# Performance work log

Measured on AMD Instinct MI355X. Metric: run time of the kernel, lower is better.

The kernel has to match this reference:

```python
import jax, jax.numpy as jnp
import numpy as np

B, S, D = 1, 2048, 2048
NH, NKV, HD = 32, 8, 64
EPS = 1e-5
SCALE = float(HD) ** 0.5


def _rope(x, cos, sin):
    # x: [b, h, s, hd]; cos/sin: [s, hd//2]; interleaved-pair rotary (executorch style)
    xr = x[..., 0::2]
    xi = x[..., 1::2]
    c = cos[None, None, :, :]
    s = sin[None, None, :, :]
    out_r = xr * c - xi * s
    out_i = xr * s + xi * c
    return jnp.stack([out_r, out_i], axis=-1).reshape(x.shape)


def _rmsnorm(x, w):
    var = jnp.mean(x * x, axis=-1, keepdims=True)
    return x * jax.lax.rsqrt(var + EPS) * w


def setup_inputs() -> dict:
    key = jax.random.key(0)
    ks = jax.random.split(key, 6)
    hidden_states = jax.random.normal(ks[0], (B, S, D), dtype=jnp.float32)
    # standard Llama rope tables, theta=10000
    inv_freq = 1.0 / (10000.0 ** (np.arange(0, HD, 2, dtype=np.float32) / HD))
    t = np.arange(S, dtype=np.float32)
    ang = np.outer(t, inv_freq)  # [S, HD//2]
    freqs_cos = jnp.asarray(np.cos(ang), dtype=jnp.float32)
    freqs_sin = jnp.asarray(np.sin(ang), dtype=jnp.float32)
    # additive causal mask [1,1,S,S]
    causal = jnp.tril(jnp.ones((S, S), dtype=bool))
    atten_mask = jnp.where(causal, 0.0, -1e9).astype(jnp.float32)[None, None]
    sd = 1.0 / np.sqrt(D)
    wq = jax.random.normal(ks[1], (NH * HD, D), dtype=jnp.float32) * sd
    wk = jax.random.normal(ks[2], (NKV * HD, D), dtype=jnp.float32) * sd
    wv = jax.random.normal(ks[3], (NKV * HD, D), dtype=jnp.float32) * sd
    wo = jax.random.normal(ks[4], (D, NH * HD), dtype=jnp.float32) * sd
    q_norm_w = jnp.ones((HD,), dtype=jnp.float32)
    k_norm_w = jnp.ones((HD,), dtype=jnp.float32)
    return dict(hidden_states=hidden_states, freqs_cos=freqs_cos, freqs_sin=freqs_sin,
                atten_mask=atten_mask, wq=wq, wk=wk, wv=wv, wo=wo,
                q_norm_w=q_norm_w, k_norm_w=k_norm_w)


def reference(hidden_states, freqs_cos, freqs_sin, atten_mask, wq, wk, wv, wo, q_norm_w, k_norm_w):
    b, s, _ = hidden_states.shape
    n_rep = NH // NKV
    # fused QKV projections (Linear: x @ W.T)
    q = (hidden_states @ wq.T).reshape(b, s, NH, HD).transpose(0, 2, 1, 3)   # [b,nh,s,hd]
    k = (hidden_states @ wk.T).reshape(b, s, NKV, HD).transpose(0, 2, 1, 3)  # [b,nkv,s,hd]
    v = (hidden_states @ wv.T).reshape(b, s, NKV, HD).transpose(0, 2, 1, 3)
    # RoPE, then QK RMSNorm (qk_norm_before_rope=False)
    q = _rope(q, freqs_cos, freqs_sin)
    k = _rope(k, freqs_cos, freqs_sin)
    q = _rmsnorm(q, q_norm_w)
    k = _rmsnorm(k, k_norm_w)
    # no KV cache (prefill): kh = k^T, vh = v, then GQA repeat
    kh = jnp.repeat(k, n_rep, axis=1)  # [b,nh,s,hd]
    vh = jnp.repeat(v, n_rep, axis=1)
    attn = jnp.einsum('bhqd,bhkd->bhqk', q, kh) / SCALE
    attn = jax.nn.softmax(attn + atten_mask, axis=-1)
    y = jnp.einsum('bhqk,bhkd->bhqd', attn, vh)
    y = y.transpose(0, 2, 1, 3).reshape(b, s, NH * HD)
    y = y @ wo.T
    # module returns (y, [kh], [vh]); kh stored transposed (b,nh,hd,s)
    return (y, kh.transpose(0, 1, 3, 2), vh)
```

## Files before the change

kernel.cpp:

```cpp
#include <hip/hip_runtime.h>
#include <cstdint>
#include <cstddef>

#define S_   2048
#define D_   2048
#define NH_  32
#define NKV_ 8
#define HD_  64

using bf16x8 = __attribute__((ext_vector_type(8))) __bf16;
using f32x4  = __attribute__((ext_vector_type(4))) float;

#define AS_GLOBAL(p) (const __attribute__((address_space(1))) void*)(p)
#define AS_LDS(p)    (__attribute__((address_space(3))) void*)(p)

__global__ __launch_bounds__(256) void cvt_all(
    const float* __restrict__ hs, const float* __restrict__ wq,
    const float* __restrict__ wk, const float* __restrict__ wv,
    const float* __restrict__ wo,
    __bf16* __restrict__ hs_bf, __bf16* __restrict__ wq_bf,
    __bf16* __restrict__ wk_bf, __bf16* __restrict__ wv_bf,
    __bf16* __restrict__ wo_bf) {
  int i = blockIdx.x * 256 + threadIdx.x;
  const float* src; __bf16* dst; int base;
  if (i < 1048576)      { src = hs; dst = hs_bf; base = 0; }
  else if (i < 2097152) { src = wq; dst = wq_bf; base = 1048576; }
  else if (i < 2359296) { src = wk; dst = wk_bf; base = 2097152; }
  else if (i < 2621440) { src = wv; dst = wv_bf; base = 2359296; }
  else                  { src = wo; dst = wo_bf; base = 2621440; }
  i -= base;
  const float4 v = reinterpret_cast<const float4*>(src)[i];
  __bf16 t[4] = {(__bf16)v.x, (__bf16)v.y, (__bf16)v.z, (__bf16)v.w};
  reinterpret_cast<uint2*>(dst)[i] = *reinterpret_cast<uint2*>(t);
}

__device__ __forceinline__ void gemm_compute_step(
    const char* ldsA, const char* ldsB, f32x4 (&acc)[4][4],
    int l15, int lg, int wm, int wn) {
  bf16x8 af[4][2], bfr[4][2];
#pragma unroll
  for (int f = 0; f < 4; ++f) {
    const int arow = wm*64 + f*16 + l15;
    const int brow = wn*64 + f*16 + l15;
#pragma unroll
    for (int ks = 0; ks < 2; ++ks) {
      af[f][ks] = *reinterpret_cast<const bf16x8*>(
          ldsA + arow*128 + (((ks*4 + lg) ^ (arow & 7)) << 4));
      bfr[f][ks] = *reinterpret_cast<const bf16x8*>(
          ldsB + brow*128 + (((ks*4 + lg) ^ (brow & 7)) << 4));
    }
  }
#pragma unroll
  for (int mf = 0; mf < 4; ++mf)
#pragma unroll
    for (int nf = 0; nf < 4; ++nf) {
      acc[mf][nf] = __builtin_amdgcn_mfma_f32_16x16x32_bf16(
          af[mf][0], bfr[nf][0], acc[mf][nf], 0, 0, 0);
      acc[mf][nf] = __builtin_amdgcn_mfma_f32_16x16x32_bf16(
          af[mf][1], bfr[nf][1], acc[mf][nf], 0, 0, 0);
    }
}

__device__ __forceinline__ void gemm_tile_128(
    const __bf16* __restrict__ A, const __bf16* __restrict__ B,
    float* __restrict__ C, int K, int N, int m0, int n0) {
  __shared__ __align__(16) char lds[2][32768];
  const int tid = threadIdx.x;
  const int l = tid & 63;
  const int w = tid >> 6;
  const int l15 = l & 15, lg = l >> 4;
  const int wm = w >> 1, wn = w & 1;

  f32x4 acc[4][4] = {};

  const int srow   = tid >> 3;
  const int schunk = (tid & 7) ^ (srow & 7);
  const __bf16* gA = A + (size_t)(m0 + srow) * K + schunk * 8;
  const __bf16* gB = B + (size_t)(n0 + srow) * K + schunk * 8;
  const int ldst = tid * 16;
  const int nt = K >> 6;

#pragma unroll
  for (int i = 0; i < 4; ++i) {
    __builtin_amdgcn_global_load_lds(AS_GLOBAL(gA + (size_t)i*32*K),
                                     AS_LDS(&lds[0][i*4096 + ldst]), 16, 0, 0);
    __builtin_amdgcn_global_load_lds(AS_GLOBAL(gB + (size_t)i*32*K),
                                     AS_LDS(&lds[0][16384 + i*4096 + ldst]), 16, 0, 0);
  }
  __syncthreads();

  int cur = 0;
  for (int t = 0; t < nt; ++t) {
    if (t + 1 < nt) {
      const int k0 = (t + 1) * 64;
      char* dA = &lds[cur ^ 1][0];
      char* dB = &lds[cur ^ 1][16384];
#pragma unroll
      for (int i = 0; i < 4; ++i) {
        __builtin_amdgcn_global_load_lds(AS_GLOBAL(gA + (size_t)i*32*K + k0),
                                         AS_LDS(dA + i*4096 + ldst), 16, 0, 0);
        __builtin_amdgcn_global_load_lds(AS_GLOBAL(gB + (size_t)i*32*K + k0),
                                         AS_LDS(dB + i*4096 + ldst), 16, 0, 0);
      }
    }
    gemm_compute_step(&lds[cur][0], &lds[cur][16384], acc, l15, lg, wm, wn);
    __syncthreads();
    cur ^= 1;
  }

#pragma unroll
  for (int mf = 0; mf < 4; ++mf)
#pragma unroll
    for (int nf = 0; nf < 4; ++nf)
#pragma unroll
      for (int r = 0; r < 4; ++r)
        C[(size_t)(m0 + wm*64 + mf*16 + lg*4 + r) * N + n0 + wn*64 + nf*16 + l15]
            = acc[mf][nf][r];
}

__device__ __forceinline__ void gemm_tile_128_d2(
    const __bf16* __restrict__ A, const __bf16* __restrict__ B,
    float* __restrict__ C, int K, int N, int m0, int n0) {
  __shared__ __align__(16) char lds[3][32768];
  const int tid = threadIdx.x;
  const int l = tid & 63;
  const int w = tid >> 6;
  const int l15 = l & 15, lg = l >> 4;
  const int wm = w >> 1, wn = w & 1;

  f32x4 acc[4][4] = {};

  const int srow   = tid >> 3;
  const int schunk = (tid & 7) ^ (srow & 7);
  const __bf16* gA = A + (size_t)(m0 + srow) * K + schunk * 8;
  const __bf16* gB = B + (size_t)(n0 + srow) * K + schunk * 8;
  const int ldst = tid * 16;
  const int nt = K >> 6;

#pragma unroll
  for (int i = 0; i < 4; ++i) {
    __builtin_amdgcn_global_load_lds(AS_GLOBAL(gA + (size_t)i*32*K),
                                     AS_LDS(&lds[0][i*4096 + ldst]), 16, 0, 0);
    __builtin_amdgcn_global_load_lds(AS_GLOBAL(gB + (size_t)i*32*K),
                                     AS_LDS(&lds[0][16384 + i*4096 + ldst]), 16, 0, 0);
  }
#pragma unroll
  for (int i = 0; i < 4; ++i) {
    __builtin_amdgcn_global_load_lds(AS_GLOBAL(gA + (size_t)i*32*K + 64),
                                     AS_LDS(&lds[1][i*4096 + ldst]), 16, 0, 0);
    __builtin_amdgcn_global_load_lds(AS_GLOBAL(gB + (size_t)i*32*K + 64),
                                     AS_LDS(&lds[1][16384 + i*4096 + ldst]), 16, 0, 0);
  }

  char* p0 = &lds[0][0];
  char* p1 = &lds[1][0];
  char* p2 = &lds[2][0];

  for (int t = 0; t < nt; ++t) {
    if (t + 1 < nt) asm volatile("s_waitcnt vmcnt(8)" ::: "memory");
    else            asm volatile("s_waitcnt vmcnt(0)" ::: "memory");
    __builtin_amdgcn_s_barrier();

    if (t + 2 < nt) {
      const int k0 = (t + 2) * 64;
#pragma unroll
      for (int i = 0; i < 4; ++i) {
        __builtin_amdgcn_global_load_lds(AS_GLOBAL(gA + (size_t)i*32*K + k0),
                                         AS_LDS(p2 + i*4096 + ldst), 16, 0, 0);
        __builtin_amdgcn_global_load_lds(AS_GLOBAL(gB + (size_t)i*32*K + k0),
                                         AS_LDS(p2 + 16384 + i*4096 + ldst), 16, 0, 0);
      }
    }

    gemm_compute_step(p0, p0 + 16384, acc, l15, lg, wm, wn);

    char* tmp = p0; p0 = p1; p1 = p2; p2 = tmp;
  }

#pragma unroll
  for (int mf = 0; mf < 4; ++mf)
#pragma unroll
    for (int nf = 0; nf < 4; ++nf)
#pragma unroll
      for (int r = 0; r < 4; ++r)
        C[(size_t)(m0 + wm*64 + mf*16 + lg*4 + r) * N + n0 + wn*64 + nf*16 + l15]
            = acc[mf][nf][r];
}

__global__ __launch_bounds__(256) void gemm_qkv(
    const __bf16* __restrict__ hs,
    const __bf16* __restrict__ wq, const __bf16* __restrict__ wk,
    const __bf16* __restrict__ wv,
    float* __restrict__ qp, float* __restrict__ kp, float* __restrict__ vp) {
  const int bx = blockIdx.x;
  const __bf16* Bm; float* Cm; int N, n0;
  if (bx < 16)      { Bm = wq; Cm = qp; N = 2048; n0 = bx * 128; }
  else if (bx < 20) { Bm = wk; Cm = kp; N = 512;  n0 = (bx - 16) * 128; }
  else              { Bm = wv; Cm = vp; N = 512;  n0 = (bx - 20) * 128; }
  gemm_tile_128(hs, Bm, Cm, 2048, N, blockIdx.y * 128, n0);
}

__global__ __launch_bounds__(256) void gemm_wo(
    const __bf16* __restrict__ ypre, const __bf16* __restrict__ wo,
    float* __restrict__ y) {
  gemm_tile_128_d2(ypre, wo, y, 2048, 2048, blockIdx.y * 128, blockIdx.x * 128);
}

__global__ __launch_bounds__(256) void rope_norm_q(
    const float* __restrict__ q, const float* __restrict__ cosT,
    const float* __restrict__ sinT, const float* __restrict__ w,
    __bf16* __restrict__ qbf) {
  const int wid  = (int)((blockIdx.x * 256 + threadIdx.x) >> 6);
  const int lane = threadIdx.x & 63;
  const int s = wid >> 5;
  const int h = wid & 31;
  const size_t idx = (size_t)s*D_ + h*HD_ + lane;
  float val = q[idx];
  const float c  = cosT[s*32 + (lane >> 1)];
  const float sn = sinT[s*32 + (lane >> 1)];
  const float partner = __shfl_xor(val, 1);
  const float ro = (lane & 1) ? fmaf(partner, sn, val*c)
                              : fmaf(val, c, -partner*sn);
  float ssq = ro * ro;
#pragma unroll
  for (int off = 32; off >= 1; off >>= 1) ssq += __shfl_xor(ssq, off);
  const float rinv = rsqrtf(ssq * (1.0f/64.0f) + 1e-5f);
  qbf[idx] = (__bf16)(ro * rinv * w[lane] * 0.180336880111120426f);
}

__global__ __launch_bounds__(256) void rope_norm_k(
    float* __restrict__ k, const float* __restrict__ cosT,
    const float* __restrict__ sinT, const float* __restrict__ w,
    __bf16* __restrict__ kbf) {
  const int wid  = (int)((blockIdx.x * 256 + threadIdx.x) >> 6);
  const int lane = threadIdx.x & 63;
  const int s   = wid >> 3;
  const int kvh = wid & 7;
  const size_t idx = (size_t)s*(NKV_*HD_) + kvh*HD_ + lane;
  float val = k[idx];
  const float c  = cosT[s*32 + (lane >> 1)];
  const float sn = sinT[s*32 + (lane >> 1)];
  const float partner = __shfl_xor(val, 1);
  const float ro = (lane & 1) ? fmaf(partner, sn, val*c)
                              : fmaf(val, c, -partner*sn);
  float ssq = ro * ro;
#pragma unroll
  for (int off = 32; off >= 1; off >>= 1) ssq += __shfl_xor(ssq, off);
  const float rinv = rsqrtf(ssq * (1.0f/64.0f) + 1e-5f);
  const float res = ro * rinv * w[lane];
  k[idx] = res;
  kbf[idx] = (__bf16)res;
}

__global__ __launch_bounds__(256) void transpose_khT(
    const float* __restrict__ kpost, float* __restrict__ khT) {
  __shared__ float tl[64][68];
  const int s0  = blockIdx.x * 64;
  const int kvh = blockIdx.y;
  const int t = threadIdx.x;
  {
    const int d0 = (t & 15) * 4;
    const int sl = t >> 4;
#pragma unroll
    for (int rep = 0; rep < 4; ++rep) {
      const int srow = sl + rep*16;
      float4 v = *reinterpret_cast<const float4*>(
          &kpost[(size_t)(s0 + srow)*(NKV_*HD_) + kvh*HD_ + d0]);
      tl[d0+0][srow]=v.x; tl[d0+1][srow]=v.y; tl[d0+2][srow]=v.z; tl[d0+3][srow]=v.w;
    }
  }
  __syncthreads();
  {
    const int d  = t >> 2;
    const int s4 = (t & 3) * 16;
#pragma unroll
    for (int c = 0; c < 4; ++c) {
      float4 v;
      v.x = tl[d][s4+c*4+0]; v.y = tl[d][s4+c*4+1];
      v.z = tl[d][s4+c*4+2]; v.w = tl[d][s4+c*4+3];
#pragma unroll
      for (int r = 0; r < 4; ++r) {
        *reinterpret_cast<float4*>(
            &khT[((size_t)(kvh*4 + r)*HD_ + d)*S_ + s0 + s4 + c*4]) = v;
      }
    }
  }
}

__global__ __launch_bounds__(256) void transpose_v(
    const float* __restrict__ vp, float* __restrict__ vh,
    __bf16* __restrict__ vtbf) {
  __shared__ float tl[64][68];
  const int s0  = blockIdx.x * 64;
  const int kvh = blockIdx.y;
  const int t = threadIdx.x;
  const int srow = t >> 2, dc = (t & 3) * 16;
  const float* src = &vp[(size_t)(s0 + srow)*(NKV_*HD_) + kvh*HD_ + dc];
  float4 a = reinterpret_cast<const float4*>(src)[0];
  float4 b = reinterpret_cast<const float4*>(src)[1];
  float4 c = reinterpret_cast<const float4*>(src)[2];
  float4 d = reinterpret_cast<const float4*>(src)[3];
  *reinterpret_cast<float4*>(&tl[srow][dc])      = a;
  *reinterpret_cast<float4*>(&tl[srow][dc + 4])  = b;
  *reinterpret_cast<float4*>(&tl[srow][dc + 8])  = c;
  *reinterpret_cast<float4*>(&tl[srow][dc + 12]) = d;
#pragma unroll
  for (int r = 0; r < 4; ++r) {
    float* dst = &vh[((size_t)(kvh*4 + r)*S_ + s0 + srow)*HD_ + dc];
    reinterpret_cast<float4*>(dst)[0] = a;
    reinterpret_cast<float4*>(dst)[1] = b;
    reinterpret_cast<float4*>(dst)[2] = c;
    reinterpret_cast<float4*>(dst)[3] = d;
  }
  __syncthreads();
  const int dr = t >> 2, sc = (t & 3) * 16;
  __bf16 vals[16];
#pragma unroll
  for (int i = 0; i < 16; ++i) vals[i] = (__bf16)tl[sc + i][dr];
  uint4* dst = reinterpret_cast<uint4*>(&vtbf[((size_t)(kvh*64 + dr))*S_ + s0 + sc]);
  dst[0] = reinterpret_cast<uint4*>(vals)[0];
  dst[1] = reinterpret_cast<uint4*>(vals)[1];
}

__device__ __forceinline__ uint pack2bf(float a, float b) {
  __bf16 x = (__bf16)a, y = (__bf16)b;
  const uint ux = (uint)*reinterpret_cast<ushort*>(&x);
  const uint uy = (uint)*reinterpret_cast<ushort*>(&y);
  return ux | (uy << 16);
}

__device__ __forceinline__ void qk_tile_T(
    const char* kldh, bf16x8 qf0, bf16x8 qf1, f32x4 (&s_)[4],
    int l15, int lg) {
  __builtin_amdgcn_s_setprio(1);
#pragma unroll
  for (int nb = 0; nb < 4; ++nb) {
    const int row = nb*16 + l15;
    const int bc  = lg*16;
    const bf16x8 kb0 = *reinterpret_cast<const bf16x8*>(
        kldh + row*128 + ((bc)      ^ ((row & 7) << 4)));
    const bf16x8 kb1 = *reinterpret_cast<const bf16x8*>(
        kldh + row*128 + ((bc + 64) ^ ((row & 7) << 4)));
    f32x4 t = f32x4{0.f, 0.f, 0.f, 0.f};
    t = __builtin_amdgcn_mfma_f32_16x16x32_bf16(kb0, qf0, t, 0, 0, 0);
    t = __builtin_amdgcn_mfma_f32_16x16x32_bf16(kb1, qf1, t, 0, 0, 0);
    s_[nb] = t;
  }
  __builtin_amdgcn_s_setprio(0);
}

__device__ __forceinline__ void softmax_pv_T(
    f32x4 (&s_)[4], float& m_, float& l_, f32x4 (&o_)[4],
    char* pldw, const char* vbase, int l15, int lg) {
  float mx = fmaxf(fmaxf(s_[0][0], s_[0][1]), fmaxf(s_[0][2], s_[0][3]));
#pragma unroll
  for (int nb = 1; nb < 4; ++nb) {
    mx = fmaxf(mx, fmaxf(fmaxf(s_[nb][0], s_[nb][1]),
                         fmaxf(s_[nb][2], s_[nb][3])));
  }
  mx = fmaxf(mx, __shfl_xor(mx, 16));
  mx = fmaxf(mx, __shfl_xor(mx, 32));
  const float mnew = fmaxf(m_, mx);
  const float scl = exp2f(m_ - mnew);
  m_ = mnew;

  const int swz = (l15 & 7) << 4;
  float ls = 0.f;
#pragma unroll
  for (int nb = 0; nb < 4; ++nb) {
    float p0 = exp2f(s_[nb][0] - mnew);
    float p1 = exp2f(s_[nb][1] - mnew);
    float p2 = exp2f(s_[nb][2] - mnew);
    float p3 = exp2f(s_[nb][3] - mnew);
    ls += (p0 + p1) + (p2 + p3);
    *reinterpret_cast<uint*>(pldw + ((l15*128 + nb*32 + lg*8)     ^ swz)) = pack2bf(p0, p1);
    *reinterpret_cast<uint*>(pldw + ((l15*128 + nb*32 + lg*8 + 4) ^ swz)) = pack2bf(p2, p3);
  }
  ls += __shfl_xor(ls, 16);
  ls += __shfl_xor(ls, 32);
  l_ = l_*scl + ls;
#pragma unroll
  for (int nb = 0; nb < 4; ++nb) {
    o_[nb][0] *= scl; o_[nb][1] *= scl; o_[nb][2] *= scl; o_[nb][3] *= scl;
  }

  const bf16x8 pb0 = *reinterpret_cast<const bf16x8*>(
      pldw + ((l15*128 + lg*16)      ^ swz));
  const bf16x8 pb1 = *reinterpret_cast<const bf16x8*>(
      pldw + ((l15*128 + lg*16 + 64) ^ swz));

  __builtin_amdgcn_s_setprio(1);
#pragma unroll
  for (int nb = 0; nb < 4; ++nb) {
    const int row = nb*16 + l15;
    const int bc  = lg*16;
    const bf16x8 v0 = *reinterpret_cast<const bf16x8*>(
        vbase + row*128 + ((bc)      ^ ((row & 7) << 4)));
    const bf16x8 v1 = *reinterpret_cast<const bf16x8*>(
        vbase + row*128 + ((bc + 64) ^ ((row & 7) << 4)));
    f32x4 t = o_[nb];
    t = __builtin_amdgcn_mfma_f32_16x16x32_bf16(v0, pb0, t, 0, 0, 0);
    t = __builtin_amdgcn_mfma_f32_16x16x32_bf16(v1, pb1, t, 0, 0, 0);
    o_[nb] = t;
  }
  __builtin_amdgcn_s_setprio(0);
}

__device__ __forceinline__ void mask_diag_T(f32x4 (&s_)[4], int l15, int lg, int wg) {
  const int qrow = wg*16 + l15;
#pragma unroll
  for (int nb = 0; nb < 4; ++nb)
#pragma unroll
    for (int r = 0; r < 4; ++r)
      if (nb*16 + lg*4 + r > qrow) s_[nb][r] = -1e30f;
}

__global__ __launch_bounds__(512, 4) void flash_attn_mfma(
    const __bf16* __restrict__ qbf, const __bf16* __restrict__ kbf,
    const __bf16* __restrict__ vtbf, __bf16* __restrict__ ypre) {
  __shared__ __align__(16) char smem[49152];

  const int h   = blockIdx.y;
  const int pi  = blockIdx.x;
  const int qbA = pi, qbB = 31 - pi;
  const int SS  = (qbB >> 1) + 1;
  const int kvh = h >> 2;
  const int tid = threadIdx.x;
  const int l   = tid & 63;
  const int w   = tid >> 6;
  const int g   = tid >> 8;
  const int wg  = w & 3;
  const int l15 = l & 15;
  const int lg  = l >> 4;

  char* kldg = smem + g*8192;
  char* vtlg = smem + 16384 + g*8192;
  char* pldw = smem + 32768 + w*2048;

  const int ts = tid & 255;
  const int j  = ts >> 2;
  const int c0 = (ts & 3) * 16;
  const int b0 = (j*128 + c0*2)      ^ ((j & 7) << 4);
  const int b1 = (j*128 + c0*2 + 16) ^ ((j & 7) << 4);
  const __bf16* ksrc = kbf  + (size_t)(g*64 + j)*(NKV_*HD_) + kvh*HD_ + c0;
  const __bf16* vsrc = vtbf + (size_t)(kvh*64 + j)*S_ + g*64 + c0;

  bf16x8 qfA0, qfA1, qfB0, qfB1;
  {
    const __bf16* qa = qbf + (size_t)(qbA*64 + wg*16 + l15)*D_ + h*HD_ + lg*8;
    qfA0 = *reinterpret_cast<const bf16x8*>(qa);
    qfA1 = *reinterpret_cast<const bf16x8*>(qa + 32);
    const __bf16* qb = qbf + (size_t)(qbB*64 + wg*16 + l15)*D_ + h*HD_ + lg*8;
    qfB0 = *reinterpret_cast<const bf16x8*>(qb);
    qfB1 = *reinterpret_cast<const bf16x8*>(qb + 32);
  }

  f32x4 oA[4], oB[4];
#pragma unroll
  for (int nb = 0; nb < 4; ++nb) {
    oA[nb] = f32x4{0.f, 0.f, 0.f, 0.f};
    oB[nb] = f32x4{0.f, 0.f, 0.f, 0.f};
  }
  float mA = -1e30f, lA = 0.f, mB = -1e30f, lB = 0.f;

  uint4 kr0 = reinterpret_cast<const uint4*>(ksrc)[0];
  uint4 kr1 = reinterpret_cast<const uint4*>(ksrc + 8)[0];
  uint4 vr0 = reinterpret_cast<const uint4*>(vsrc)[0];
  uint4 vr1 = reinterpret_cast<const uint4*>(vsrc + 8)[0];

  for (int st = 0; st < SS; ++st) {
    __syncthreads();
    *reinterpret_cast<uint4*>(kldg + b0) = kr0;
    *reinterpret_cast<uint4*>(kldg + b1) = kr1;
    *reinterpret_cast<uint4*>(vtlg + b0) = vr0;
    *reinterpret_cast<uint4*>(vtlg + b1) = vr1;
    __syncthreads();

    if (st + 1 < SS) {
      const __bf16* kn = ksrc + (size_t)(st + 1)*128*(NKV_*HD_);
      const __bf16* vn = vsrc + (size_t)(st + 1)*128;
      kr0 = reinterpret_cast<const uint4*>(kn)[0];
      kr1 = reinterpret_cast<const uint4*>(kn + 8)[0];
      vr0 = reinterpret_cast<const uint4*>(vn)[0];
      vr1 = reinterpret_cast<const uint4*>(vn + 8)[0];
    }

    const int kt = 2*st + g;
    if (kt <= qbB) {
      f32x4 s_[4];
      qk_tile_T(kldg, qfB0, qfB1, s_, l15, lg);
      if (kt == qbB) mask_diag_T(s_, l15, lg, wg);
      softmax_pv_T(s_, mB, lB, oB, pldw, vtlg, l15, lg);
    }
    if (kt <= qbA) {
      f32x4 s_[4];
      qk_tile_T(kldg, qfA0, qfA1, s_, l15, lg);
      if (kt == qbA) mask_diag_T(s_, l15, lg, wg);
      softmax_pv_T(s_, mA, lA, oA, pldw, vtlg, l15, lg);
    }
  }

  float* ox = reinterpret_cast<float*>(smem);
  float* ml = reinterpret_cast<float*>(smem + 20480);
  float* po = ox + (wg*64 + l)*17;
  float* pm = ml + (wg*64 + l)*9;

  __syncthreads();
  if (g == 1) {
#pragma unroll
    for (int nb = 0; nb < 4; ++nb)
#pragma unroll
      for (int r = 0; r < 4; ++r) po[nb*4 + r] = oB[nb][r];
    pm[0] = mB; pm[1] = lB;
  }
  __syncthreads();
  if (g == 0) {
    const float m1 = pm[0], l1 = pm[1];
    const float m = fmaxf(mB, m1);
    const float s0 = exp2f(mB - m), s1 = exp2f(m1 - m);
    lB = lB*s0 + l1*s1;
#pragma unroll
    for (int nb = 0; nb < 4; ++nb)
#pragma unroll
      for (int r = 0; r < 4; ++r)
        oB[nb][r] = oB[nb][r]*s0 + po[nb*4 + r]*s1;
  }
  __syncthreads();
  if (g == 1) {
#pragma unroll
    for (int nb = 0; nb < 4; ++nb)
#pragma unroll
      for (int r = 0; r < 4; ++r) po[nb*4 + r] = oA[nb][r];
    pm[0] = mA; pm[1] = lA;
  }
  __syncthreads();
  if (g == 0) {
    const float m1 = pm[0], l1 = pm[1];
    const float m = fmaxf(mA, m1);
    const float s0 = exp2f(mA - m), s1 = exp2f(m1 - m);
    lA = lA*s0 + l1*s1;
#pragma unroll
    for (int nb = 0; nb < 4; ++nb)
#pragma unroll
      for (int r = 0; r < 4; ++r)
        oA[nb][r] = oA[nb][r]*s0 + po[nb*4 + r]*s1;

    const float rlA = 1.0f / lA, rlB = 1.0f / lB;
    const size_t rowA = (size_t)(qbA*64 + wg*16 + l15)*D_ + h*HD_;
    const size_t rowB = (size_t)(qbB*64 + wg*16 + l15)*D_ + h*HD_;
#pragma unroll
    for (int nb = 0; nb < 4; ++nb) {
      uint2 pa, pb;
      pa.x = pack2bf(oA[nb][0]*rlA, oA[nb][1]*rlA);
      pa.y = pack2bf(oA[nb][2]*rlA, oA[nb][3]*rlA);
      pb.x = pack2bf(oB[nb][0]*rlB, oB[nb][1]*rlB);
      pb.y = pack2bf(oB[nb][2]*rlB, oB[nb][3]*rlB);
      *reinterpret_cast<uint2*>(&ypre[rowA + nb*16 + lg*4]) = pa;
      *reinterpret_cast<uint2*>(&ypre[rowB + nb*16 + lg*4]) = pb;
    }
  }
}

extern "C" void kernel_launch(void* const* d_in, const int* in_sizes, int n_in,
                              void* d_out, int out_size, void* d_ws, size_t ws_size,
                              hipStream_t stream) {
  (void)in_sizes; (void)n_in; (void)out_size;
  const float* hs   = (const float*)d_in[0];
  const float* fcos = (const float*)d_in[1];
  const float* fsin = (const float*)d_in[2];
  const float* wq = (const float*)d_in[4];
  const float* wk = (const float*)d_in[5];
  const float* wv = (const float*)d_in[6];
  const float* wo = (const float*)d_in[7];
  const float* qw = (const float*)d_in[8];
  const float* kw = (const float*)d_in[9];

  float* out = (float*)d_out;
  float* y   = out;
  float* khT = out + 4194304;
  float* vh  = out + 8388608;

  __bf16* qbf   = (__bf16*)y;
  __bf16* kbf   = (__bf16*)((char*)y + 8*1024*1024);
  __bf16* vtbf  = (__bf16*)((char*)y + 10*1024*1024);
  __bf16* hs_bf = (__bf16*)khT;
  __bf16* wq_bf = (__bf16*)((char*)khT + 8*1024*1024);
  __bf16* wk_bf = (__bf16*)vh;
  __bf16* wv_bf = (__bf16*)((char*)vh + 2*1024*1024);

  const size_t need = (size_t)40 * 1024 * 1024;
  if (ws_size < need) return;
  char* ws = (char*)d_ws;
  float*  qp      = (float*)(ws);
  float*  kp      = (float*)(ws + 16*1024*1024);
  float*  vp      = (float*)(ws + 20*1024*1024);
  __bf16* ypre_bf = (__bf16*)(ws + 24*1024*1024);
  __bf16* wo_bf   = (__bf16*)(ws + 32*1024*1024);

  cvt_all<<<14336, 256, 0, stream>>>(hs, wq, wk, wv, wo,
                                     hs_bf, wq_bf, wk_bf, wv_bf, wo_bf);

  gemm_qkv<<<dim3(24, 16), 256, 0, stream>>>(hs_bf, wq_bf, wk_bf, wv_bf, qp, kp, vp);

  rope_norm_q<<<16384, 256, 0, stream>>>(qp, fcos, fsin, qw, qbf);
  rope_norm_k<<< 4096, 256, 0, stream>>>(kp, fcos, fsin, kw, kbf);

  transpose_khT<<<dim3(32, 8), 256, 0, stream>>>(kp, khT);
  transpose_v<<<dim3(32, 8), 256, 0, stream>>>(vp, vh, vtbf);

  flash_attn_mfma<<<dim3(16, 32), 512, 0, stream>>>(qbf, kbf, vtbf, ypre_bf);

  gemm_wo<<<dim3(16, 16), 256, 0, stream>>>(ypre_bf, wo_bf, y);
}
```

Before: 154.2 us.

## Store QKV projections as bf16 and double-buffer K/V tiles in attention

The QKV GEMM now writes its outputs in bf16 instead of fp32. The rope/norm and transpose kernels read bf16, which halves intermediate traffic, and khT is now built from the already-normalized bf16 keys. The flash attention kernel double-buffers its K/V LDS tiles, so each step needs one barrier instead of two. In exchange, the fp32 kh and vh outputs lose precision because they pass through bf16, and the attention kernel's LDS use grows from 48KB to 80KB, which may lower occupancy under launch_bounds(512,4).

```diff
diff --git a/kernel.cpp b/kernel.cpp
--- a/kernel.cpp
+++ b/kernel.cpp
@@ -13,6 +13,10 @@
 
 #define AS_GLOBAL(p) (const __attribute__((address_space(1))) void*)(p)
 #define AS_LDS(p)    (__attribute__((address_space(3))) void*)(p)
+
+__device__ __forceinline__ float b2f(uint u) {
+  union { uint u; float f; } c; c.u = u << 16; return c.f;
+}
 
 __global__ __launch_bounds__(256) void cvt_all(
     const float* __restrict__ hs, const float* __restrict__ wq,
@@ -61,9 +65,9 @@
     }
 }
 
-__device__ __forceinline__ void gemm_tile_128(
+__device__ __forceinline__ void gemm_tile_128_bf(
     const __bf16* __restrict__ A, const __bf16* __restrict__ B,
-    float* __restrict__ C, int K, int N, int m0, int n0) {
+    __bf16* __restrict__ C, int K, int N, int m0, int n0) {
   __shared__ __align__(16) char lds[2][32768];
   const int tid = threadIdx.x;
   const int l = tid & 63;
@@ -115,7 +119,7 @@
 #pragma unroll
       for (int r = 0; r < 4; ++r)
         C[(size_t)(m0 + wm*64 + mf*16 + lg*4 + r) * N + n0 + wn*64 + nf*16 + l15]
-            = acc[mf][nf][r];
+            = (__bf16)acc[mf][nf][r];
 }
 
 __device__ __forceinline__ void gemm_tile_128_d2(
@@ -191,13 +195,13 @@
     const __bf16* __restrict__ hs,
     const __bf16* __restrict__ wq, const __bf16* __restrict__ wk,
     const __bf16* __restrict__ wv,
-    float* __restrict__ qp, float* __restrict__ kp, float* __restrict__ vp) {
+    __bf16* __restrict__ qp, __bf16* __restrict__ kp, __bf16* __restrict__ vp) {
   const int bx = blockIdx.x;
-  const __bf16* Bm; float* Cm; int N, n0;
+  const __bf16* Bm; __bf16* Cm; int N, n0;
   if (bx < 16)      { Bm = wq; Cm = qp; N = 2048; n0 = bx * 128; }
   else if (bx < 20) { Bm = wk; Cm = kp; N = 512;  n0 = (bx - 16) * 128; }
   else              { Bm = wv; Cm = vp; N = 512;  n0 = (bx - 20) * 128; }
-  gemm_tile_128(hs, Bm, Cm, 2048, N, blockIdx.y * 128, n0);
+  gemm_tile_128_bf(hs, Bm, Cm, 2048, N, blockIdx.y * 128, n0);
 }
 
 __global__ __launch_bounds__(256) void gemm_wo(
@@ -207,7 +211,7 @@
 }
 
 __global__ __launch_bounds__(256) void rope_norm_q(
-    const float* __restrict__ q, const float* __restrict__ cosT,
+    const __bf16* __restrict__ q, const float* __restrict__ cosT,
     const float* __restrict__ sinT, const float* __restrict__ w,
     __bf16* __restrict__ qbf) {
   const int wid  = (int)((blockIdx.x * 256 + threadIdx.x) >> 6);
@@ -215,7 +219,7 @@
   const int s = wid >> 5;
   const int h = wid & 31;
   const size_t idx = (size_t)s*D_ + h*HD_ + lane;
-  float val = q[idx];
+  float val = (float)q[idx];
   const float c  = cosT[s*32 + (lane >> 1)];
   const float sn = sinT[s*32 + (lane >> 1)];
   const float partner = __shfl_xor(val, 1);
@@ -229,7 +233,7 @@
 }
 
 __global__ __launch_bounds__(256) void rope_norm_k(
-    float* __restrict__ k, const float* __restrict__ cosT,
+    const __bf16* __restrict__ k, const float* __restrict__ cosT,
     const float* __restrict__ sinT, const float* __restrict__ w,
     __bf16* __restrict__ kbf) {
   const int wid  = (int)((blockIdx.x * 256 + threadIdx.x) >> 6);
@@ -237,7 +241,7 @@
   const int s   = wid >> 3;
   const int kvh = wid & 7;
   const size_t idx = (size_t)s*(NKV_*HD_) + kvh*HD_ + lane;
-  float val = k[idx];
+  float val = (float)k[idx];
   const float c  = cosT[s*32 + (lane >> 1)];
   const float sn = sinT[s*32 + (lane >> 1)];
   const float partner = __shfl_xor(val, 1);
@@ -247,13 +251,11 @@
 #pragma unroll
   for (int off = 32; off >= 1; off >>= 1) ssq += __shfl_xor(ssq, off);
   const float rinv = rsqrtf(ssq * (1.0f/64.0f) + 1e-5f);
-  const float res = ro * rinv * w[lane];
-  k[idx] = res;
-  kbf[idx] = (__bf16)res;
+  kbf[idx] = (__bf16)(ro * rinv * w[lane]);
 }
 
 __global__ __launch_bounds__(256) void transpose_khT(
-    const float* __restrict__ kpost, float* __restrict__ khT) {
+    const __bf16* __restrict__ kpost, float* __restrict__ khT) {
   __shared__ float tl[64][68];
   const int s0  = blockIdx.x * 64;
   const int kvh = blockIdx.y;
@@ -264,9 +266,12 @@
 #pragma unroll
     for (int rep = 0; rep < 4; ++rep) {
       const int srow = sl + rep*16;
-      float4 v = *reinterpret_cast<const float4*>(
+      const uint2 v = *reinterpret_cast<const uint2*>(
           &kpost[(size_t)(s0 + srow)*(NKV_*HD_) + kvh*HD_ + d0]);
-      tl[d0+0][srow]=v.x; tl[d0+1][srow]=v.y; tl[d0+2][srow]=v.z; tl[d0+3][srow]=v.w;
+      tl[d0+0][srow] = b2f(v.x & 0xffff);
+      tl[d0+1][srow] = b2f(v.x >> 16);
+      tl[d0+2][srow] = b2f(v.y & 0xffff);
+      tl[d0+3][srow] = b2f(v.y >> 16);
     }
   }
   __syncthreads();
@@ -288,29 +293,31 @@
 }
 
 __global__ __launch_bounds__(256) void transpose_v(
-    const float* __restrict__ vp, float* __restrict__ vh,
+    const __bf16* __restrict__ vp, float* __restrict__ vh,
     __bf16* __restrict__ vtbf) {
   __shared__ float tl[64][68];
   const int s0  = blockIdx.x * 64;
   const int kvh = blockIdx.y;
   const int t = threadIdx.x;
   const int srow = t >> 2, dc = (t & 3) * 16;
-  const float* src = &vp[(size_t)(s0 + srow)*(NKV_*HD_) + kvh*HD_ + dc];
-  float4 a = reinterpret_cast<const float4*>(src)[0];
-  float4 b = reinterpret_cast<const float4*>(src)[1];
-  float4 c = reinterpret_cast<const float4*>(src)[2];
-  float4 d = reinterpret_cast<const float4*>(src)[3];
-  *reinterpret_cast<float4*>(&tl[srow][dc])      = a;
-  *reinterpret_cast<float4*>(&tl[srow][dc + 4])  = b;
-  *reinterpret_cast<float4*>(&tl[srow][dc + 8])  = c;
-  *reinterpret_cast<float4*>(&tl[srow][dc + 12]) = d;
+  const __bf16* src = &vp[(size_t)(s0 + srow)*(NKV_*HD_) + kvh*HD_ + dc];
+  const uint4 a = reinterpret_cast<const uint4*>(src)[0];
+  const uint4 b = reinterpret_cast<const uint4*>(src)[1];
+  float f[16];
+  f[0]=b2f(a.x&0xffff); f[1]=b2f(a.x>>16); f[2]=b2f(a.y&0xffff); f[3]=b2f(a.y>>16);
+  f[4]=b2f(a.z&0xffff); f[5]=b2f(a.z>>16); f[6]=b2f(a.w&0xffff); f[7]=b2f(a.w>>16);
+  f[8]=b2f(b.x&0xffff); f[9]=b2f(b.x>>16); f[10]=b2f(b.y&0xffff); f[11]=b2f(b.y>>16);
+  f[12]=b2f(b.z&0xffff); f[13]=b2f(b.z>>16); f[14]=b2f(b.w&0xffff); f[15]=b2f(b.w>>16);
+#pragma unroll
+  for (int i = 0; i < 16; ++i) tl[srow][dc + i] = f[i];
 #pragma unroll
   for (int r = 0; r < 4; ++r) {
     float* dst = &vh[((size_t)(kvh*4 + r)*S_ + s0 + srow)*HD_ + dc];
-    reinterpret_cast<float4*>(dst)[0] = a;
-    reinterpret_cast<float4*>(dst)[1] = b;
-    reinterpret_cast<float4*>(dst)[2] = c;
-    reinterpret_cast<float4*>(dst)[3] = d;
+#pragma unroll
+    for (int cc = 0; cc < 4; ++cc) {
+      float4 v4 = {f[cc*4+0], f[cc*4+1], f[cc*4+2], f[cc*4+3]};
+      reinterpret_cast<float4*>(dst)[cc] = v4;
+    }
   }
   __syncthreads();
   const int dr = t >> 2, sc = (t & 3) * 16;
@@ -418,7 +425,7 @@
 __global__ __launch_bounds__(512, 4) void flash_attn_mfma(
     const __bf16* __restrict__ qbf, const __bf16* __restrict__ kbf,
     const __bf16* __restrict__ vtbf, __bf16* __restrict__ ypre) {
-  __shared__ __align__(16) char smem[49152];
+  __shared__ __align__(16) char smem[81920];
 
   const int h   = blockIdx.y;
   const int pi  = blockIdx.x;
@@ -433,9 +440,9 @@
   const int l15 = l & 15;
   const int lg  = l >> 4;
 
-  char* kldg = smem + g*8192;
-  char* vtlg = smem + 16384 + g*8192;
-  char* pldw = smem + 32768 + w*2048;
+  char* kb[2] = { smem + (g*2 + 0)*8192, smem + (g*2 + 1)*8192 };
+  char* vb[2] = { smem + 32768 + (g*2 + 0)*8192, smem + 32768 + (g*2 + 1)*8192 };
+  char* pldw  = smem + 65536 + w*2048;
 
   const int ts = tid & 255;
   const int j  = ts >> 2;
@@ -467,37 +474,51 @@
   uint4 kr1 = reinterpret_cast<const uint4*>(ksrc + 8)[0];
   uint4 vr0 = reinterpret_cast<const uint4*>(vsrc)[0];
   uint4 vr1 = reinterpret_cast<const uint4*>(vsrc + 8)[0];
+  *reinterpret_cast<uint4*>(kb[0] + b0) = kr0;
+  *reinterpret_cast<uint4*>(kb[0] + b1) = kr1;
+  *reinterpret_cast<uint4*>(vb[0] + b0) = vr0;
+  *reinterpret_cast<uint4*>(vb[0] + b1) = vr1;
+  if (SS > 1) {
+    const __bf16* kn = ksrc + (size_t)128*(NKV_*HD_);
+    const __bf16* vn = vsrc + 128;
+    kr0 = reinterpret_cast<const uint4*>(kn)[0];
+    kr1 = reinterpret_cast<const uint4*>(kn + 8)[0];
+    vr0 = reinterpret_cast<const uint4*>(vn)[0];
+    vr1 = reinterpret_cast<const uint4*>(vn + 8)[0];
+  }
+  __syncthreads();
 
   for (int st = 0; st < SS; ++st) {
-    __syncthreads();
-    *reinterpret_cast<uint4*>(kldg + b0) = kr0;
-    *reinterpret_cast<uint4*>(kldg + b1) = kr1;
-    *reinterpret_cast<uint4*>(vtlg + b0) = vr0;
-    *reinterpret_cast<uint4*>(vtlg + b1) = vr1;
-    __syncthreads();
-
+    const int cur = st & 1;
     if (st + 1 < SS) {
-      const __bf16* kn = ksrc + (size_t)(st + 1)*128*(NKV_*HD_);
-      const __bf16* vn = vsrc + (size_t)(st + 1)*128;
-      kr0 = reinterpret_cast<const uint4*>(kn)[0];
-      kr1 = reinterpret_cast<const uint4*>(kn + 8)[0];
-      vr0 = reinterpret_cast<const uint4*>(vn)[0];
-      vr1 = reinterpret_cast<const uint4*>(vn + 8)[0];
+      *reinterpret_cast<uint4*>(kb[cur ^ 1] + b0) = kr0;
+      *reinterpret_cast<uint4*>(kb[cur ^ 1] + b1) = kr1;
+      *reinterpret_cast<uint4*>(vb[cur ^ 1] + b0) = vr0;
+      *reinterpret_cast<uint4*>(vb[cur ^ 1] + b1) = vr1;
+      if (st + 2 < SS) {
+        const __bf16* kn = ksrc + (size_t)(st + 2)*128*(NKV_*HD_);
+        const __bf16* vn = vsrc + (size_t)(st + 2)*128;
+        kr0 = reinterpret_cast<const uint4*>(kn)[0];
+        kr1 = reinterpret_cast<const uint4*>(kn + 8)[0];
+        vr0 = reinterpret_cast<const uint4*>(vn)[0];
+        vr1 = reinterpret_cast<const uint4*>(vn + 8)[0];
+      }
     }
 
     const int kt = 2*st + g;
     if (kt <= qbB) {
       f32x4 s_[4];
-      qk_tile_T(kldg, qfB0, qfB1, s_, l15, lg);
+      qk_tile_T(kb[cur], qfB0, qfB1, s_, l15, lg);
       if (kt == qbB) mask_diag_T(s_, l15, lg, wg);
-      softmax_pv_T(s_, mB, lB, oB, pldw, vtlg, l15, lg);
+      softmax_pv_T(s_, mB, lB, oB, pldw, vb[cur], l15, lg);
     }
     if (kt <= qbA) {
       f32x4 s_[4];
-      qk_tile_T(kldg, qfA0, qfA1, s_, l15, lg);
+      qk_tile_T(kb[cur], qfA0, qfA1, s_, l15, lg);
       if (kt == qbA) mask_diag_T(s_, l15, lg, wg);
-      softmax_pv_T(s_, mA, lA, oA, pldw, vtlg, l15, lg);
-    }
+      softmax_pv_T(s_, mA, lA, oA, pldw, vb[cur], l15, lg);
+    }
+    __syncthreads();
   }
 
   float* ox = reinterpret_cast<float*>(smem);
@@ -505,7 +526,6 @@
   float* po = ox + (wg*64 + l)*17;
   float* pm = ml + (wg*64 + l)*9;
 
-  __syncthreads();
   if (g == 1) {
 #pragma unroll
     for (int nb = 0; nb < 4; ++nb)
@@ -591,22 +611,23 @@
   const size_t need = (size_t)40 * 1024 * 1024;
   if (ws_size < need) return;
   char* ws = (char*)d_ws;
-  float*  qp      = (float*)(ws);
-  float*  kp      = (float*)(ws + 16*1024*1024);
-  float*  vp      = (float*)(ws + 20*1024*1024);
-  __bf16* ypre_bf = (__bf16*)(ws + 24*1024*1024);
-  __bf16* wo_bf   = (__bf16*)(ws + 32*1024*1024);
+  __bf16* qp_bf   = (__bf16*)(ws);
+  __bf16* kp_bf   = (__bf16*)(ws + 8*1024*1024);
+  __bf16* vp_bf   = (__bf16*)(ws + 10*1024*1024);
+  __bf16* ypre_bf = (__bf16*)(ws + 12*1024*1024);
+  __bf16* wo_bf   = (__bf16*)(ws + 20*1024*1024);
 
   cvt_all<<<14336, 256, 0, stream>>>(hs, wq, wk, wv, wo,
                                      hs_bf, wq_bf, wk_bf, wv_bf, wo_bf);
 
-  gemm_qkv<<<dim3(24, 16), 256, 0, stream>>>(hs_bf, wq_bf, wk_bf, wv_bf, qp, kp, vp);
-
-  rope_norm_q<<<16384, 256, 0, stream>>>(qp, fcos, fsin, qw, qbf);
-  rope_norm_k<<< 4096, 256, 0, stream>>>(kp, fcos, fsin, kw, kbf);
-
-  transpose_khT<<<dim3(32, 8), 256, 0, stream>>>(kp, khT);
-  transpose_v<<<dim3(32, 8), 256, 0, stream>>>(vp, vh, vtbf);
+  gemm_qkv<<<dim3(24, 16), 256, 0, stream>>>(hs_bf, wq_bf, wk_bf, wv_bf,
+                                             qp_bf, kp_bf, vp_bf);
+
+  rope_norm_q<<<16384, 256, 0, stream>>>(qp_bf, fcos, fsin, qw, qbf);
+  rope_norm_k<<< 4096, 256, 0, stream>>>(kp_bf, fcos, fsin, kw, kbf);
+
+  transpose_khT<<<dim3(32, 8), 256, 0, stream>>>(kbf, khT);
+  transpose_v<<<dim3(32, 8), 256, 0, stream>>>(vp_bf, vh, vtbf);
 
   flash_attn_mfma<<<dim3(16, 32), 512, 0, stream>>>(qbf, kbf, vtbf, ypre_bf);
 
```

New measurement: 181.5 us. +17.7%, slower.
